# Optimization experiments

Measured on AMD Instinct MI355X. Metric: run time of the kernel, lower is better.

The kernel has to match this reference:

```python
import jax, jax.numpy as jnp
import numpy as np

V_IN, E, H, V_OUT = 32000, 512, 1024, 50257


def setup_inputs() -> dict:
    key = jax.random.key(0)
    ks = jax.random.split(key, 12)
    g = lambda k, shape: (jax.random.normal(k, shape, dtype=jnp.float32) * 0.05)
    return {
        "state": jax.random.randint(ks[0], (1, 2048), 0, V_IN),
        "max_len": 512,
        "emb": g(ks[1], (V_IN, E)),
        "enc_Wih": g(ks[2], (4 * H, E)),
        "enc_Whh": g(ks[3], (4 * H, H)),
        "enc_bih": g(ks[4], (4 * H,)),
        "enc_bhh": g(ks[5], (4 * H,)),
        "dec_Wih": g(ks[6], (4 * H, 1)),
        "dec_Whh": g(ks[7], (4 * H, H)),
        "dec_bih": g(ks[8], (4 * H,)),
        "dec_bhh": g(ks[9], (4 * H,)),
        "Wout": g(ks[10], (V_OUT, H)),
        "bout": g(ks[11], (V_OUT,)),
    }


def _lstm_cell(h, c, gates):
    # PyTorch gate order: i, f, g, o
    i, f, g, o = jnp.split(gates, 4)
    i = jax.nn.sigmoid(i)
    f = jax.nn.sigmoid(f)
    g = jnp.tanh(g)
    o = jax.nn.sigmoid(o)
    c = f * c + i * g
    h = o * jnp.tanh(c)
    return h, c


def reference(state, max_len, emb, enc_Wih, enc_Whh, enc_bih, enc_bhh,
              dec_Wih, dec_Whh, dec_bih, dec_bhh, Wout, bout):
    hdim = enc_Whh.shape[1]
    # ---- encoder: embed tokens, run LSTM over seq (batch = 1) ----
    xs = emb[state[0]]  # [S, E]
    enc_b = enc_bih + enc_bhh

    def enc_step(carry, x):
        h, c = carry
        gates = enc_Wih @ x + enc_Whh @ h + enc_b  # [4H]
        return _lstm_cell(h, c, gates), None

    z = jnp.zeros((hdim,), dtype=emb.dtype)
    (h, c), _ = jax.lax.scan(enc_step, (z, z), xs)

    # ---- decoder: input is always zeros(1,1,1), so Wih contributes 0 ----
    dec_b = dec_bih + dec_bhh + dec_Wih[:, 0] * 0.0

    def dec_step(carry, _):
        h, c = carry
        gates = dec_Whh @ h + dec_b
        h, c = _lstm_cell(h, c, gates)
        probs = jax.nn.softmax(Wout @ h + bout)  # [V_out]
        return (h, c), probs

    _, probs = jax.lax.scan(dec_step, (h, c), None, length=max_len)
    return probs[None]  # [1, max_len, V_out]
```

## Files before the change

kernel.cpp:

```cpp
#include <hip/hip_runtime.h>
#include <stdint.h>
#include <math.h>


typedef __attribute__((ext_vector_type(8))) short short8;
typedef __attribute__((ext_vector_type(4))) float f32x4;
typedef unsigned long long u64;

#define HD 1024
#define ED 512
#define TPB 256
#define NWG 256
#define SENT64 0x7F7F7F7F7F7F7F7FULL

#define AGT __HIP_MEMORY_SCOPE_AGENT
#define RLX __ATOMIC_RELAXED

__device__ __forceinline__ unsigned short f2bf(float f) {
  union { float f; unsigned u; } x; x.f = f;
  unsigned u = x.u;
  u += 0x7fffu + ((u >> 16) & 1u);
  return (unsigned short)(u >> 16);
}
__device__ __forceinline__ float sigmf(float x) { return 1.0f / (1.0f + expf(-x)); }

__global__ __launch_bounds__(TPB)
void rnn_kernel(const int* __restrict__ state,
                const float* __restrict__ emb,
                const float* __restrict__ encWih,
                const float* __restrict__ encWhh,
                const float* __restrict__ encbih,
                const float* __restrict__ encbhh,
                const float* __restrict__ decWhh,
                const float* __restrict__ decbih,
                const float* __restrict__ decbhh,
                u64* __restrict__ hlines,
                unsigned short* __restrict__ Adec,
                int S, int T) {
  __shared__ __align__(16) float vec[1536];
  __shared__ float gsh[16];

  const int tid = threadIdx.x;
  const int wg  = blockIdx.x;
  const int row = tid >> 4;
  const int c   = tid & 15;
  const int grow = (row & 3) * HD + (wg << 2) + (row >> 2);

  float4 w[24];
#pragma unroll
  for (int j = 0; j < 16; ++j)
    w[j] = *(const float4*)&encWhh[(size_t)grow * HD + 4 * (c + 16 * j)];
#pragma unroll
  for (int j = 16; j < 24; ++j)
    w[j] = *(const float4*)&encWih[(size_t)grow * ED + 4 * (c + 16 * j) - HD];
  float breg = encbih[grow] + encbhh[grow];

  float ccell = 0.0f;

  for (int t = 0; t < S + T; ++t) {
    const bool dec = (t >= S);
    if (t == S) {
#pragma unroll
      for (int j = 0; j < 16; ++j)
        w[j] = *(const float4*)&decWhh[(size_t)grow * HD + 4 * (c + 16 * j)];
      breg = decbih[grow] + decbhh[grow];
    }

    if (t == 0) {
      *(float4*)&vec[4 * tid] = make_float4(0.f, 0.f, 0.f, 0.f);
      if (tid >= 128) {
        int tok = state[0];
        *(float4*)&vec[HD + 4 * (tid - 128)] =
            *(const float4*)&emb[(size_t)tok * ED + 4 * (tid - 128)];
      }
    } else {
      float4 xv;
      const bool havex = (!dec) && (tid >= 128);
      if (havex) {
        int tok = state[t];
        xv = *(const float4*)&emb[(size_t)tok * ED + 4 * (tid - 128)];
      }
      const u64* L = hlines + (((size_t)(t & 3) << 8) + tid) * 8;
      u64 d0, d1;
      do {
        d0 = __hip_atomic_load(&L[0], RLX, AGT);
        d1 = __hip_atomic_load(&L[1], RLX, AGT);
      } while (d0 == SENT64 || d1 == SENT64);
      union { u64 u; float2 f; } a, b;
      a.u = d0; b.u = d1;
      *(float2*)&vec[4 * tid + 0] = a.f;
      *(float2*)&vec[4 * tid + 2] = b.f;
      if (havex) *(float4*)&vec[HD + 4 * (tid - 128)] = xv;
    }
    if (tid == 0) {
      u64* C = hlines + (((size_t)((t + 2) & 3) << 8) + wg) * 8;
      __hip_atomic_store(&C[0], SENT64, RLX, AGT);
      __hip_atomic_store(&C[1], SENT64, RLX, AGT);
    }
    __syncthreads();

    float a0 = (c == 0) ? breg : 0.0f, a1 = 0.f, a2 = 0.f, a3 = 0.f;
    if (!dec) {
#pragma unroll
      for (int j = 0; j < 24; j += 4) {
        float4 v0 = *(const float4*)&vec[4 * (c + 16 * (j + 0))];
        float4 v1 = *(const float4*)&vec[4 * (c + 16 * (j + 1))];
        float4 v2 = *(const float4*)&vec[4 * (c + 16 * (j + 2))];
        float4 v3 = *(const float4*)&vec[4 * (c + 16 * (j + 3))];
        float4 w0 = w[j + 0], w1 = w[j + 1], w2 = w[j + 2], w3 = w[j + 3];
        a0 = fmaf(w0.x, v0.x, fmaf(w0.y, v0.y, fmaf(w0.z, v0.z, fmaf(w0.w, v0.w, a0))));
        a1 = fmaf(w1.x, v1.x, fmaf(w1.y, v1.y, fmaf(w1.z, v1.z, fmaf(w1.w, v1.w, a1))));
        a2 = fmaf(w2.x, v2.x, fmaf(w2.y, v2.y, fmaf(w2.z, v2.z, fmaf(w2.w, v2.w, a2))));
        a3 = fmaf(w3.x, v3.x, fmaf(w3.y, v3.y, fmaf(w3.z, v3.z, fmaf(w3.w, v3.w, a3))));
      }
    } else {
#pragma unroll
      for (int j = 0; j < 16; j += 4) {
        float4 v0 = *(const float4*)&vec[4 * (c + 16 * (j + 0))];
        float4 v1 = *(const float4*)&vec[4 * (c + 16 * (j + 1))];
        float4 v2 = *(const float4*)&vec[4 * (c + 16 * (j + 2))];
        float4 v3 = *(const float4*)&vec[4 * (c + 16 * (j + 3))];
        float4 w0 = w[j + 0], w1 = w[j + 1], w2 = w[j + 2], w3 = w[j + 3];
        a0 = fmaf(w0.x, v0.x, fmaf(w0.y, v0.y, fmaf(w0.z, v0.z, fmaf(w0.w, v0.w, a0))));
        a1 = fmaf(w1.x, v1.x, fmaf(w1.y, v1.y, fmaf(w1.z, v1.z, fmaf(w1.w, v1.w, a1))));
        a2 = fmaf(w2.x, v2.x, fmaf(w2.y, v2.y, fmaf(w2.z, v2.z, fmaf(w2.w, v2.w, a2))));
        a3 = fmaf(w3.x, v3.x, fmaf(w3.y, v3.y, fmaf(w3.z, v3.z, fmaf(w3.w, v3.w, a3))));
      }
    }
    float acc = (a0 + a1) + (a2 + a3);
    acc += __shfl_xor(acc, 1);
    acc += __shfl_xor(acc, 2);
    acc += __shfl_xor(acc, 4);
    acc += __shfl_xor(acc, 8);
    if (c == 0) gsh[row] = acc;
    __syncthreads();

    float hv = 0.0f;
    if (tid < 4) {
      float gi = gsh[(tid << 2) + 0];
      float gf = gsh[(tid << 2) + 1];
      float gg = gsh[(tid << 2) + 2];
      float go = gsh[(tid << 2) + 3];
      float iv = sigmf(gi), fv = sigmf(gf), gv = tanhf(gg), ov = sigmf(go);
      ccell = fv * ccell + iv * gv;
      hv = ov * tanhf(ccell);
      if (dec) Adec[(size_t)(t - S) * HD + (wg << 2) + tid] = f2bf(hv);
    }
    if (tid < 64) {
      float h0 = __shfl(hv, 0), h1 = __shfl(hv, 1);
      float h2 = __shfl(hv, 2), h3 = __shfl(hv, 3);
      if (tid == 0) {
        asm volatile("s_waitcnt vmcnt(0)" ::: "memory");
        u64* P = hlines + (((size_t)((t + 1) & 3) << 8) + wg) * 8;
        union { float2 f; u64 u; } p0, p1;
        p0.f = make_float2(h0, h1); p1.f = make_float2(h2, h3);
        __hip_atomic_store(&P[0], p0.u, RLX, AGT);
        __hip_atomic_store(&P[1], p1.u, RLX, AGT);
      }
    }
  }
}

#define AST 56

__global__ __launch_bounds__(TPB)
void out_gemm(const unsigned short* __restrict__ Adec,
              const float* __restrict__ Wout,
              const float* __restrict__ bout,
              float* __restrict__ out,
              int V) {
  __shared__ __align__(16) unsigned short Alds[512 * AST];
  const int tid  = threadIdx.x;
  const int wv   = tid >> 6;
  const int lane = tid & 63;
  const int col  = lane & 15;
  const int quad = lane >> 4;
  const int v0   = blockIdx.x * 64;

  f32x4 acc[4][8];
#pragma unroll
  for (int bt = 0; bt < 4; ++bt)
#pragma unroll
    for (int tt = 0; tt < 8; ++tt)
      acc[bt][tt] = (f32x4){0.f, 0.f, 0.f, 0.f};

  for (int k0 = 0; k0 < HD; k0 += 32) {
    __syncthreads();
#pragma unroll
    for (int i = 0; i < 8; ++i) {
      int id = tid + (i << 8);
      int rt = id >> 2, c4 = id & 3;
      uint4 d = *(const uint4*)(Adec + rt * HD + k0 + (c4 << 3));
      *(uint4*)&Alds[rt * AST + (c4 << 3)] = d;
    }
    __syncthreads();
    short8 bf[4];
#pragma unroll
    for (int bt = 0; bt < 4; ++bt) {
      int v = v0 + (bt << 4) + col;
      if (v >= V) v = V - 1;
      const float4* wp = (const float4*)(Wout + (size_t)v * HD + k0 + (quad << 3));
      float4 w0 = wp[0], w1 = wp[1];
      short8 b;
      b[0] = (short)f2bf(w0.x); b[1] = (short)f2bf(w0.y);
      b[2] = (short)f2bf(w0.z); b[3] = (short)f2bf(w0.w);
      b[4] = (short)f2bf(w1.x); b[5] = (short)f2bf(w1.y);
      b[6] = (short)f2bf(w1.z); b[7] = (short)f2bf(w1.w);
      bf[bt] = b;
    }
#pragma unroll
    for (int tt = 0; tt < 8; ++tt) {
      int trow = (wv << 7) + (tt << 4) + col;
      short8 af = *(const short8*)&Alds[trow * AST + (quad << 3)];
#pragma unroll
      for (int bt = 0; bt < 4; ++bt)
        acc[bt][tt] = __builtin_amdgcn_mfma_f32_16x16x32_bf16(af, bf[bt], acc[bt][tt], 0, 0, 0);
    }
  }
#pragma unroll
  for (int bt = 0; bt < 4; ++bt) {
    int v = v0 + (bt << 4) + col;
    if (v < V) {
      float bb = bout[v];
#pragma unroll
      for (int tt = 0; tt < 8; ++tt) {
        int tb = (wv << 7) + (tt << 4) + (quad << 2);
        f32x4 a = acc[bt][tt];
        out[(size_t)(tb + 0) * V + v] = a[0] + bb;
        out[(size_t)(tb + 1) * V + v] = a[1] + bb;
        out[(size_t)(tb + 2) * V + v] = a[2] + bb;
        out[(size_t)(tb + 3) * V + v] = a[3] + bb;
      }
    }
  }
}

__global__ __launch_bounds__(TPB)
void softmax_rows(float* __restrict__ out, int V) {
  float* rowp = out + (size_t)blockIdx.x * V;
  __shared__ float red[8];
  const int tid = threadIdx.x;

  float m = -1e30f;
  for (int v = tid; v < V; v += TPB) m = fmaxf(m, rowp[v]);
#pragma unroll
  for (int off = 32; off >= 1; off >>= 1) m = fmaxf(m, __shfl_xor(m, off));
  if ((tid & 63) == 0) red[tid >> 6] = m;
  __syncthreads();
  if (tid == 0) red[4] = fmaxf(fmaxf(red[0], red[1]), fmaxf(red[2], red[3]));
  __syncthreads();
  m = red[4];

  float s = 0.0f;
  for (int v = tid; v < V; v += TPB) {
    float e = expf(rowp[v] - m);
    rowp[v] = e;
    s += e;
  }
#pragma unroll
  for (int off = 32; off >= 1; off >>= 1) s += __shfl_xor(s, off);
  if ((tid & 63) == 0) red[tid >> 6] = s;
  __syncthreads();
  if (tid == 0) red[5] = red[0] + red[1] + red[2] + red[3];
  __syncthreads();
  float inv = 1.0f / red[5];
  for (int v = tid; v < V; v += TPB) rowp[v] *= inv;
}

extern "C" void kernel_launch(void* const* d_in, const int* in_sizes, int n_in,
                              void* d_out, int out_size, void* d_ws, size_t ws_size,
                              hipStream_t stream) {
  const int*   state  = (const int*)d_in[0];
  const float* emb    = (const float*)d_in[2];
  const float* encWih = (const float*)d_in[3];
  const float* encWhh = (const float*)d_in[4];
  const float* encbih = (const float*)d_in[5];
  const float* encbhh = (const float*)d_in[6];
  const float* decWhh = (const float*)d_in[8];
  const float* decbih = (const float*)d_in[9];
  const float* decbhh = (const float*)d_in[10];
  const float* Wout   = (const float*)d_in[11];
  const float* bout   = (const float*)d_in[12];
  float*       out    = (float*)d_out;

  const int S = in_sizes[0];
  const int V = in_sizes[12];
  const int T = out_size / V;

  hipMemsetAsync(d_ws, 0x7F, 65536, stream);
  u64*            hlines = (u64*)d_ws;
  unsigned short* Adec   = (unsigned short*)((char*)d_ws + 65536);

  rnn_kernel<<<NWG, TPB, 0, stream>>>(state, emb, encWih, encWhh, encbih, encbhh,
                                      decWhh, decbih, decbhh, hlines, Adec, S, T);
  int nvb = (V + 63) / 64;
  out_gemm<<<nvb, TPB, 0, stream>>>(Adec, Wout, bout, out, V);
  softmax_rows<<<T, TPB, 0, stream>>>(out, V);
}
```

Baseline: 8.155 ms.

## Restructure persistent LSTM kernel: one hidden unit per wave, fewer workgroups

Reorganizes the persistent RNN kernel so each 64-lane wave owns one hidden unit and computes all four gates, with 128 workgroups of 512 threads instead of 256 of 256. The cross-wave shared-memory gate exchange and the second barrier round trip are gone; gate activations are computed redundantly in every lane after a full-wave shuffle reduction. It also prefetches the next token's embedding one step ahead, publishes h as individual 32-bit words with per-word sentinels instead of 64-bit lines, and uses fast exp/reciprocal approximations for sigmoid and tanh. The aim is to shorten the per-timestep critical path of the grid-wide handoff. In exchange the sentinel polling now checks four words per load, and the approximate activations may lose accuracy.

```diff
diff --git a/kernel.cpp b/kernel.cpp
--- a/kernel.cpp
+++ b/kernel.cpp
@@ -10,8 +10,10 @@
 #define HD 1024
 #define ED 512
 #define TPB 256
-#define NWG 256
-#define SENT64 0x7F7F7F7F7F7F7F7FULL
+#define RNN_TPB 512
+#define RNN_NWG 128
+#define UPW 8
+#define SENT32 0x7F7F7F7Fu
 
 #define AGT __HIP_MEMORY_SCOPE_AGENT
 #define RLX __ATOMIC_RELAXED
@@ -22,9 +24,11 @@
   u += 0x7fffu + ((u >> 16) & 1u);
   return (unsigned short)(u >> 16);
 }
-__device__ __forceinline__ float sigmf(float x) { return 1.0f / (1.0f + expf(-x)); }
-
-__global__ __launch_bounds__(TPB)
+__device__ __forceinline__ float frcp(float x) { return __builtin_amdgcn_rcpf(x); }
+__device__ __forceinline__ float fsig(float x) { return frcp(1.0f + __expf(-x)); }
+__device__ __forceinline__ float ftanh(float x) { return 1.0f - 2.0f * frcp(1.0f + __expf(2.0f * x)); }
+
+__global__ __launch_bounds__(RNN_TPB)
 void rnn_kernel(const int* __restrict__ state,
                 const float* __restrict__ emb,
                 const float* __restrict__ encWih,
@@ -34,130 +38,129 @@
                 const float* __restrict__ decWhh,
                 const float* __restrict__ decbih,
                 const float* __restrict__ decbhh,
-                u64* __restrict__ hlines,
+                unsigned int* __restrict__ hbuf,
                 unsigned short* __restrict__ Adec,
                 int S, int T) {
-  __shared__ __align__(16) float vec[1536];
-  __shared__ float gsh[16];
+  __shared__ __align__(16) float vec[HD + ED];
 
   const int tid = threadIdx.x;
   const int wg  = blockIdx.x;
-  const int row = tid >> 4;
-  const int c   = tid & 15;
-  const int grow = (row & 3) * HD + (wg << 2) + (row >> 2);
-
-  float4 w[24];
-#pragma unroll
-  for (int j = 0; j < 16; ++j)
-    w[j] = *(const float4*)&encWhh[(size_t)grow * HD + 4 * (c + 16 * j)];
-#pragma unroll
-  for (int j = 16; j < 24; ++j)
-    w[j] = *(const float4*)&encWih[(size_t)grow * ED + 4 * (c + 16 * j) - HD];
-  float breg = encbih[grow] + encbhh[grow];
-
-  float ccell = 0.0f;
+  const int w   = tid >> 6;
+  const int c   = tid & 63;
+  const int u   = wg * UPW + w;
+
+  float4 wh[4][4];
+  float4 wx[4][2];
+  float4 br;
+#pragma unroll
+  for (int g = 0; g < 4; ++g) {
+    const size_t rb = (size_t)(g * HD + u);
+#pragma unroll
+    for (int j = 0; j < 4; ++j)
+      wh[g][j] = *(const float4*)&encWhh[rb * HD + 4 * (c + 64 * j)];
+#pragma unroll
+    for (int j = 0; j < 2; ++j)
+      wx[g][j] = *(const float4*)&encWih[rb * ED + 4 * (c + 64 * j)];
+  }
+  br.x = encbih[0 * HD + u] + encbhh[0 * HD + u];
+  br.y = encbih[1 * HD + u] + encbhh[1 * HD + u];
+  br.z = encbih[2 * HD + u] + encbhh[2 * HD + u];
+  br.w = encbih[3 * HD + u] + encbhh[3 * HD + u];
+
+  float4 xreg;
+  if (tid >= 256 && tid < 384) {
+    int tok = state[0];
+    xreg = *(const float4*)&emb[(size_t)tok * ED + 4 * (tid - 256)];
+  }
+
+  float cs = 0.0f;
 
   for (int t = 0; t < S + T; ++t) {
     const bool dec = (t >= S);
     if (t == S) {
 #pragma unroll
-      for (int j = 0; j < 16; ++j)
-        w[j] = *(const float4*)&decWhh[(size_t)grow * HD + 4 * (c + 16 * j)];
-      breg = decbih[grow] + decbhh[grow];
-    }
-
-    if (t == 0) {
-      *(float4*)&vec[4 * tid] = make_float4(0.f, 0.f, 0.f, 0.f);
-      if (tid >= 128) {
-        int tok = state[0];
-        *(float4*)&vec[HD + 4 * (tid - 128)] =
-            *(const float4*)&emb[(size_t)tok * ED + 4 * (tid - 128)];
-      }
-    } else {
-      float4 xv;
-      const bool havex = (!dec) && (tid >= 128);
-      if (havex) {
-        int tok = state[t];
-        xv = *(const float4*)&emb[(size_t)tok * ED + 4 * (tid - 128)];
-      }
-      const u64* L = hlines + (((size_t)(t & 3) << 8) + tid) * 8;
-      u64 d0, d1;
-      do {
-        d0 = __hip_atomic_load(&L[0], RLX, AGT);
-        d1 = __hip_atomic_load(&L[1], RLX, AGT);
-      } while (d0 == SENT64 || d1 == SENT64);
-      union { u64 u; float2 f; } a, b;
-      a.u = d0; b.u = d1;
-      *(float2*)&vec[4 * tid + 0] = a.f;
-      *(float2*)&vec[4 * tid + 2] = b.f;
-      if (havex) *(float4*)&vec[HD + 4 * (tid - 128)] = xv;
-    }
-    if (tid == 0) {
-      u64* C = hlines + (((size_t)((t + 2) & 3) << 8) + wg) * 8;
-      __hip_atomic_store(&C[0], SENT64, RLX, AGT);
-      __hip_atomic_store(&C[1], SENT64, RLX, AGT);
+      for (int g = 0; g < 4; ++g) {
+        const size_t rb = (size_t)(g * HD + u);
+#pragma unroll
+        for (int j = 0; j < 4; ++j)
+          wh[g][j] = *(const float4*)&decWhh[rb * HD + 4 * (c + 64 * j)];
+      }
+      br.x = decbih[0 * HD + u] + decbhh[0 * HD + u];
+      br.y = decbih[1 * HD + u] + decbhh[1 * HD + u];
+      br.z = decbih[2 * HD + u] + decbhh[2 * HD + u];
+      br.w = decbih[3 * HD + u] + decbhh[3 * HD + u];
+    }
+
+    if (tid < 256) {
+      if (t == 0) {
+        *(float4*)&vec[4 * tid] = make_float4(0.f, 0.f, 0.f, 0.f);
+      } else {
+        const u64* L = (const u64*)hbuf + (((size_t)(t & 3)) << 9) + tid * 2;
+        u64 d0, d1;
+        do {
+          d0 = __hip_atomic_load(&L[0], RLX, AGT);
+          d1 = __hip_atomic_load(&L[1], RLX, AGT);
+        } while ((unsigned)d0 == SENT32 || (unsigned)(d0 >> 32) == SENT32 ||
+                 (unsigned)d1 == SENT32 || (unsigned)(d1 >> 32) == SENT32);
+        union { u64 u[2]; float4 f; } p;
+        p.u[0] = d0; p.u[1] = d1;
+        *(float4*)&vec[4 * tid] = p.f;
+      }
+    } else if (tid < 384) {
+      if (!dec) {
+        *(float4*)&vec[HD + 4 * (tid - 256)] = xreg;
+        if (t + 1 < S) {
+          int tok = state[t + 1];
+          xreg = *(const float4*)&emb[(size_t)tok * ED + 4 * (tid - 256)];
+        }
+      }
     }
     __syncthreads();
 
-    float a0 = (c == 0) ? breg : 0.0f, a1 = 0.f, a2 = 0.f, a3 = 0.f;
+    if (c == 0)
+      __hip_atomic_store(&hbuf[(size_t)((t + 2) & 3) * HD + u], SENT32, RLX, AGT);
+
+    float a0 = 0.f, a1 = 0.f, a2 = 0.f, a3 = 0.f;
+#pragma unroll
+    for (int j = 0; j < 4; ++j) {
+      float4 v = *(const float4*)&vec[4 * (c + 64 * j)];
+      a0 = fmaf(wh[0][j].x, v.x, fmaf(wh[0][j].y, v.y, fmaf(wh[0][j].z, v.z, fmaf(wh[0][j].w, v.w, a0))));
+      a1 = fmaf(wh[1][j].x, v.x, fmaf(wh[1][j].y, v.y, fmaf(wh[1][j].z, v.z, fmaf(wh[1][j].w, v.w, a1))));
+      a2 = fmaf(wh[2][j].x, v.x, fmaf(wh[2][j].y, v.y, fmaf(wh[2][j].z, v.z, fmaf(wh[2][j].w, v.w, a2))));
+      a3 = fmaf(wh[3][j].x, v.x, fmaf(wh[3][j].y, v.y, fmaf(wh[3][j].z, v.z, fmaf(wh[3][j].w, v.w, a3))));
+    }
     if (!dec) {
 #pragma unroll
-      for (int j = 0; j < 24; j += 4) {
-        float4 v0 = *(const float4*)&vec[4 * (c + 16 * (j + 0))];
-        float4 v1 = *(const float4*)&vec[4 * (c + 16 * (j + 1))];
-        float4 v2 = *(const float4*)&vec[4 * (c + 16 * (j + 2))];
-        float4 v3 = *(const float4*)&vec[4 * (c + 16 * (j + 3))];
-        float4 w0 = w[j + 0], w1 = w[j + 1], w2 = w[j + 2], w3 = w[j + 3];
-        a0 = fmaf(w0.x, v0.x, fmaf(w0.y, v0.y, fmaf(w0.z, v0.z, fmaf(w0.w, v0.w, a0))));
-        a1 = fmaf(w1.x, v1.x, fmaf(w1.y, v1.y, fmaf(w1.z, v1.z, fmaf(w1.w, v1.w, a1))));
-        a2 = fmaf(w2.x, v2.x, fmaf(w2.y, v2.y, fmaf(w2.z, v2.z, fmaf(w2.w, v2.w, a2))));
-        a3 = fmaf(w3.x, v3.x, fmaf(w3.y, v3.y, fmaf(w3.z, v3.z, fmaf(w3.w, v3.w, a3))));
-      }
-    } else {
-#pragma unroll
-      for (int j = 0; j < 16; j += 4) {
-        float4 v0 = *(const float4*)&vec[4 * (c + 16 * (j + 0))];
-        float4 v1 = *(const float4*)&vec[4 * (c + 16 * (j + 1))];
-        float4 v2 = *(const float4*)&vec[4 * (c + 16 * (j + 2))];
-        float4 v3 = *(const float4*)&vec[4 * (c + 16 * (j + 3))];
-        float4 w0 = w[j + 0], w1 = w[j + 1], w2 = w[j + 2], w3 = w[j + 3];
-        a0 = fmaf(w0.x, v0.x, fmaf(w0.y, v0.y, fmaf(w0.z, v0.z, fmaf(w0.w, v0.w, a0))));
-        a1 = fmaf(w1.x, v1.x, fmaf(w1.y, v1.y, fmaf(w1.z, v1.z, fmaf(w1.w, v1.w, a1))));
-        a2 = fmaf(w2.x, v2.x, fmaf(w2.y, v2.y, fmaf(w2.z, v2.z, fmaf(w2.w, v2.w, a2))));
-        a3 = fmaf(w3.x, v3.x, fmaf(w3.y, v3.y, fmaf(w3.z, v3.z, fmaf(w3.w, v3.w, a3))));
-      }
-    }
-    float acc = (a0 + a1) + (a2 + a3);
-    acc += __shfl_xor(acc, 1);
-    acc += __shfl_xor(acc, 2);
-    acc += __shfl_xor(acc, 4);
-    acc += __shfl_xor(acc, 8);
-    if (c == 0) gsh[row] = acc;
+      for (int j = 0; j < 2; ++j) {
+        float4 v = *(const float4*)&vec[HD + 4 * (c + 64 * j)];
+        a0 = fmaf(wx[0][j].x, v.x, fmaf(wx[0][j].y, v.y, fmaf(wx[0][j].z, v.z, fmaf(wx[0][j].w, v.w, a0))));
+        a1 = fmaf(wx[1][j].x, v.x, fmaf(wx[1][j].y, v.y, fmaf(wx[1][j].z, v.z, fmaf(wx[1][j].w, v.w, a1))));
+        a2 = fmaf(wx[2][j].x, v.x, fmaf(wx[2][j].y, v.y, fmaf(wx[2][j].z, v.z, fmaf(wx[2][j].w, v.w, a2))));
+        a3 = fmaf(wx[3][j].x, v.x, fmaf(wx[3][j].y, v.y, fmaf(wx[3][j].z, v.z, fmaf(wx[3][j].w, v.w, a3))));
+      }
+    }
+#pragma unroll
+    for (int off = 1; off < 64; off <<= 1) {
+      a0 += __shfl_xor(a0, off);
+      a1 += __shfl_xor(a1, off);
+      a2 += __shfl_xor(a2, off);
+      a3 += __shfl_xor(a3, off);
+    }
+
+    float iv = fsig(a0 + br.x);
+    float fv = fsig(a1 + br.y);
+    float gv = ftanh(a2 + br.z);
+    float ov = fsig(a3 + br.w);
+    cs = fv * cs + iv * gv;
+    float hv = ov * ftanh(cs);
+
+    if (c == 0) {
+      asm volatile("s_waitcnt vmcnt(0)" ::: "memory");
+      union { float f; unsigned u; } x; x.f = hv;
+      __hip_atomic_store(&hbuf[(size_t)((t + 1) & 3) * HD + u], x.u, RLX, AGT);
+      if (dec) Adec[(size_t)(t - S) * HD + u] = f2bf(hv);
+    }
     __syncthreads();
-
-    float hv = 0.0f;
-    if (tid < 4) {
-      float gi = gsh[(tid << 2) + 0];
-      float gf = gsh[(tid << 2) + 1];
-      float gg = gsh[(tid << 2) + 2];
-      float go = gsh[(tid << 2) + 3];
-      float iv = sigmf(gi), fv = sigmf(gf), gv = tanhf(gg), ov = sigmf(go);
-      ccell = fv * ccell + iv * gv;
-      hv = ov * tanhf(ccell);
-      if (dec) Adec[(size_t)(t - S) * HD + (wg << 2) + tid] = f2bf(hv);
-    }
-    if (tid < 64) {
-      float h0 = __shfl(hv, 0), h1 = __shfl(hv, 1);
-      float h2 = __shfl(hv, 2), h3 = __shfl(hv, 3);
-      if (tid == 0) {
-        asm volatile("s_waitcnt vmcnt(0)" ::: "memory");
-        u64* P = hlines + (((size_t)((t + 1) & 3) << 8) + wg) * 8;
-        union { float2 f; u64 u; } p0, p1;
-        p0.f = make_float2(h0, h1); p1.f = make_float2(h2, h3);
-        __hip_atomic_store(&P[0], p0.u, RLX, AGT);
-        __hip_atomic_store(&P[1], p1.u, RLX, AGT);
-      }
-    }
   }
 }
 
@@ -287,12 +290,12 @@
   const int V = in_sizes[12];
   const int T = out_size / V;
 
-  hipMemsetAsync(d_ws, 0x7F, 65536, stream);
-  u64*            hlines = (u64*)d_ws;
-  unsigned short* Adec   = (unsigned short*)((char*)d_ws + 65536);
-
-  rnn_kernel<<<NWG, TPB, 0, stream>>>(state, emb, encWih, encWhh, encbih, encbhh,
-                                      decWhh, decbih, decbhh, hlines, Adec, S, T);
+  hipMemsetAsync(d_ws, 0x7F, 16384, stream);
+  unsigned int*   hbuf = (unsigned int*)d_ws;
+  unsigned short* Adec = (unsigned short*)((char*)d_ws + 65536);
+
+  rnn_kernel<<<RNN_NWG, RNN_TPB, 0, stream>>>(state, emb, encWih, encWhh, encbih, encbhh,
+                                              decWhh, decbih, decbhh, hbuf, Adec, S, T);
   int nvb = (V + 63) / 64;
   out_gemm<<<nvb, TPB, 0, stream>>>(Adec, Wout, bout, out, V);
   softmax_rows<<<T, TPB, 0, stream>>>(out, V);
```

Result: slower. 8.441 ms (+3.5%).

## Remove second barrier and pack hidden-state exchange into dense per-unit words

Applied to the files above, without the earlier changes.

Each wavefront now computes one hidden unit's gates by shuffling the four gate sums within the wave, which removes the second __syncthreads and the shared gate array. The LDS vector buffer is double-buffered so the next step's writes cannot race with current reads. The cross-workgroup exchange changes from padded 64-byte lines per workgroup to a dense 32-bit slot per unit, each polled against a sentinel, which cuts the memset size and the number of lines touched. Fast exp/rcp approximations replace expf and tanhf. The trade-offs are more independent atomic stores per workgroup and slightly lower precision.

```diff
diff --git a/kernel.cpp b/kernel.cpp
--- a/kernel.cpp
+++ b/kernel.cpp
@@ -11,7 +11,7 @@
 #define ED 512
 #define TPB 256
 #define NWG 256
-#define SENT64 0x7F7F7F7F7F7F7F7FULL
+#define SENT32 0x7F7F7F7Fu
 
 #define AGT __HIP_MEMORY_SCOPE_AGENT
 #define RLX __ATOMIC_RELAXED
@@ -22,7 +22,9 @@
   u += 0x7fffu + ((u >> 16) & 1u);
   return (unsigned short)(u >> 16);
 }
-__device__ __forceinline__ float sigmf(float x) { return 1.0f / (1.0f + expf(-x)); }
+__device__ __forceinline__ float frcp(float x) { return __builtin_amdgcn_rcpf(x); }
+__device__ __forceinline__ float fsig(float x) { return frcp(1.0f + __expf(-x)); }
+__device__ __forceinline__ float ftanh(float x) { return 1.0f - 2.0f * frcp(1.0f + __expf(2.0f * x)); }
 
 __global__ __launch_bounds__(TPB)
 void rnn_kernel(const int* __restrict__ state,
@@ -34,17 +36,19 @@
                 const float* __restrict__ decWhh,
                 const float* __restrict__ decbih,
                 const float* __restrict__ decbhh,
-                u64* __restrict__ hlines,
+                unsigned int* __restrict__ hbuf,
                 unsigned short* __restrict__ Adec,
                 int S, int T) {
-  __shared__ __align__(16) float vec[1536];
-  __shared__ float gsh[16];
-
-  const int tid = threadIdx.x;
-  const int wg  = blockIdx.x;
-  const int row = tid >> 4;
-  const int c   = tid & 15;
+  __shared__ __align__(16) float vec[2][HD + ED];
+
+  const int tid  = threadIdx.x;
+  const int wg   = blockIdx.x;
+  const int row  = tid >> 4;
+  const int c    = tid & 15;
+  const int u    = tid >> 6;
+  const int lane = tid & 63;
   const int grow = (row & 3) * HD + (wg << 2) + (row >> 2);
+  const int gu   = (wg << 2) + u;
 
   float4 w[24];
 #pragma unroll
@@ -55,7 +59,7 @@
     w[j] = *(const float4*)&encWih[(size_t)grow * ED + 4 * (c + 16 * j) - HD];
   float breg = encbih[grow] + encbhh[grow];
 
-  float ccell = 0.0f;
+  float cs = 0.0f;
 
   for (int t = 0; t < S + T; ++t) {
     const bool dec = (t >= S);
@@ -66,11 +70,13 @@
       breg = decbih[grow] + decbhh[grow];
     }
 
+    float* vb = vec[t & 1];
+
     if (t == 0) {
-      *(float4*)&vec[4 * tid] = make_float4(0.f, 0.f, 0.f, 0.f);
+      *(float4*)&vb[4 * tid] = make_float4(0.f, 0.f, 0.f, 0.f);
       if (tid >= 128) {
         int tok = state[0];
-        *(float4*)&vec[HD + 4 * (tid - 128)] =
+        *(float4*)&vb[HD + 4 * (tid - 128)] =
             *(const float4*)&emb[(size_t)tok * ED + 4 * (tid - 128)];
       }
     } else {
@@ -80,33 +86,31 @@
         int tok = state[t];
         xv = *(const float4*)&emb[(size_t)tok * ED + 4 * (tid - 128)];
       }
-      const u64* L = hlines + (((size_t)(t & 3) << 8) + tid) * 8;
+      const u64* L = (const u64*)hbuf + (((size_t)(t & 3)) << 9) + (tid << 1);
       u64 d0, d1;
       do {
         d0 = __hip_atomic_load(&L[0], RLX, AGT);
         d1 = __hip_atomic_load(&L[1], RLX, AGT);
-      } while (d0 == SENT64 || d1 == SENT64);
-      union { u64 u; float2 f; } a, b;
-      a.u = d0; b.u = d1;
-      *(float2*)&vec[4 * tid + 0] = a.f;
-      *(float2*)&vec[4 * tid + 2] = b.f;
-      if (havex) *(float4*)&vec[HD + 4 * (tid - 128)] = xv;
-    }
-    if (tid == 0) {
-      u64* C = hlines + (((size_t)((t + 2) & 3) << 8) + wg) * 8;
-      __hip_atomic_store(&C[0], SENT64, RLX, AGT);
-      __hip_atomic_store(&C[1], SENT64, RLX, AGT);
+      } while ((unsigned)d0 == SENT32 || (unsigned)(d0 >> 32) == SENT32 ||
+               (unsigned)d1 == SENT32 || (unsigned)(d1 >> 32) == SENT32);
+      union { u64 u[2]; float4 f; } p;
+      p.u[0] = d0; p.u[1] = d1;
+      *(float4*)&vb[4 * tid] = p.f;
+      if (havex) *(float4*)&vb[HD + 4 * (tid - 128)] = xv;
     }
     __syncthreads();
+
+    if (lane == 0)
+      __hip_atomic_store(&hbuf[(size_t)((t + 2) & 3) * HD + gu], SENT32, RLX, AGT);
 
     float a0 = (c == 0) ? breg : 0.0f, a1 = 0.f, a2 = 0.f, a3 = 0.f;
     if (!dec) {
 #pragma unroll
       for (int j = 0; j < 24; j += 4) {
-        float4 v0 = *(const float4*)&vec[4 * (c + 16 * (j + 0))];
-        float4 v1 = *(const float4*)&vec[4 * (c + 16 * (j + 1))];
-        float4 v2 = *(const float4*)&vec[4 * (c + 16 * (j + 2))];
-        float4 v3 = *(const float4*)&vec[4 * (c + 16 * (j + 3))];
+        float4 v0 = *(const float4*)&vb[4 * (c + 16 * (j + 0))];
+        float4 v1 = *(const float4*)&vb[4 * (c + 16 * (j + 1))];
+        float4 v2 = *(const float4*)&vb[4 * (c + 16 * (j + 2))];
+        float4 v3 = *(const float4*)&vb[4 * (c + 16 * (j + 3))];
         float4 w0 = w[j + 0], w1 = w[j + 1], w2 = w[j + 2], w3 = w[j + 3];
         a0 = fmaf(w0.x, v0.x, fmaf(w0.y, v0.y, fmaf(w0.z, v0.z, fmaf(w0.w, v0.w, a0))));
         a1 = fmaf(w1.x, v1.x, fmaf(w1.y, v1.y, fmaf(w1.z, v1.z, fmaf(w1.w, v1.w, a1))));
@@ -116,10 +120,10 @@
     } else {
 #pragma unroll
       for (int j = 0; j < 16; j += 4) {
-        float4 v0 = *(const float4*)&vec[4 * (c + 16 * (j + 0))];
-        float4 v1 = *(const float4*)&vec[4 * (c + 16 * (j + 1))];
-        float4 v2 = *(const float4*)&vec[4 * (c + 16 * (j + 2))];
-        float4 v3 = *(const float4*)&vec[4 * (c + 16 * (j + 3))];
+        float4 v0 = *(const float4*)&vb[4 * (c + 16 * (j + 0))];
+        float4 v1 = *(const float4*)&vb[4 * (c + 16 * (j + 1))];
+        float4 v2 = *(const float4*)&vb[4 * (c + 16 * (j + 2))];
+        float4 v3 = *(const float4*)&vb[4 * (c + 16 * (j + 3))];
         float4 w0 = w[j + 0], w1 = w[j + 1], w2 = w[j + 2], w3 = w[j + 3];
         a0 = fmaf(w0.x, v0.x, fmaf(w0.y, v0.y, fmaf(w0.z, v0.z, fmaf(w0.w, v0.w, a0))));
         a1 = fmaf(w1.x, v1.x, fmaf(w1.y, v1.y, fmaf(w1.z, v1.z, fmaf(w1.w, v1.w, a1))));
@@ -132,31 +136,20 @@
     acc += __shfl_xor(acc, 2);
     acc += __shfl_xor(acc, 4);
     acc += __shfl_xor(acc, 8);
-    if (c == 0) gsh[row] = acc;
-    __syncthreads();
-
-    float hv = 0.0f;
-    if (tid < 4) {
-      float gi = gsh[(tid << 2) + 0];
-      float gf = gsh[(tid << 2) + 1];
-      float gg = gsh[(tid << 2) + 2];
-      float go = gsh[(tid << 2) + 3];
-      float iv = sigmf(gi), fv = sigmf(gf), gv = tanhf(gg), ov = sigmf(go);
-      ccell = fv * ccell + iv * gv;
-      hv = ov * tanhf(ccell);
-      if (dec) Adec[(size_t)(t - S) * HD + (wg << 2) + tid] = f2bf(hv);
-    }
-    if (tid < 64) {
-      float h0 = __shfl(hv, 0), h1 = __shfl(hv, 1);
-      float h2 = __shfl(hv, 2), h3 = __shfl(hv, 3);
-      if (tid == 0) {
-        asm volatile("s_waitcnt vmcnt(0)" ::: "memory");
-        u64* P = hlines + (((size_t)((t + 1) & 3) << 8) + wg) * 8;
-        union { float2 f; u64 u; } p0, p1;
-        p0.f = make_float2(h0, h1); p1.f = make_float2(h2, h3);
-        __hip_atomic_store(&P[0], p0.u, RLX, AGT);
-        __hip_atomic_store(&P[1], p1.u, RLX, AGT);
-      }
+
+    float gi = __shfl(acc, 0);
+    float gf = __shfl(acc, 16);
+    float gg = __shfl(acc, 32);
+    float go = __shfl(acc, 48);
+    float iv = fsig(gi), fv = fsig(gf), gv = ftanh(gg), ov = fsig(go);
+    cs = fv * cs + iv * gv;
+    float hv = ov * ftanh(cs);
+
+    if (lane == 0) {
+      asm volatile("s_waitcnt vmcnt(0)" ::: "memory");
+      union { float f; unsigned u; } x; x.f = hv;
+      __hip_atomic_store(&hbuf[(size_t)((t + 1) & 3) * HD + gu], x.u, RLX, AGT);
+      if (dec) Adec[(size_t)(t - S) * HD + gu] = f2bf(hv);
     }
   }
 }
@@ -287,12 +280,12 @@
   const int V = in_sizes[12];
   const int T = out_size / V;
 
-  hipMemsetAsync(d_ws, 0x7F, 65536, stream);
-  u64*            hlines = (u64*)d_ws;
-  unsigned short* Adec   = (unsigned short*)((char*)d_ws + 65536);
+  hipMemsetAsync(d_ws, 0x7F, 16384, stream);
+  unsigned int*   hbuf = (unsigned int*)d_ws;
+  unsigned short* Adec = (unsigned short*)((char*)d_ws + 65536);
 
   rnn_kernel<<<NWG, TPB, 0, stream>>>(state, emb, encWih, encWhh, encbih, encbhh,
-                                      decWhh, decbih, decbhh, hlines, Adec, S, T);
+                                      decWhh, decbih, decbhh, hbuf, Adec, S, T);
   int nvb = (V + 63) / 64;
   out_gemm<<<nvb, TPB, 0, stream>>>(Adec, Wout, bout, out, V);
   softmax_rows<<<T, TPB, 0, stream>>>(out, V);
```

Result: slower. 10.75 ms (+31.8%).
